# Kernel tuning notes

Hardware: AMD Instinct MI355X
Metric: run time of the kernel (lower is better)

The kernel has to match this reference:

```python
import jax, jax.numpy as jnp
import numpy as np


def _warp(x, flow):
    """Backward bilinear warp (grid_sample equivalent, zeros padding).

    x:    [B, C, H, W] feature frame
    flow: [B, 2, H, W] per-pixel motion vector (x, y) in pixels
    Samples x at (px + flow_x, py + flow_y) with bilinear interpolation;
    out-of-bounds samples contribute zero (padding_mode='zeros').
    """
    B, C, H, W = x.shape
    ys, xs = jnp.meshgrid(jnp.arange(H, dtype=x.dtype), jnp.arange(W, dtype=x.dtype), indexing='ij')
    gx = xs[None] + flow[:, 0]  # [B, H, W] sample x coords
    gy = ys[None] + flow[:, 1]  # [B, H, W] sample y coords
    x0 = jnp.floor(gx)
    y0 = jnp.floor(gy)
    wx = gx - x0
    wy = gy - y0
    flat = x.reshape(B, C, H * W)

    def corner(xi, yi, w):
        valid = (xi >= 0) & (xi <= W - 1) & (yi >= 0) & (yi <= H - 1)
        xc = jnp.clip(xi, 0, W - 1).astype(jnp.int32)
        yc = jnp.clip(yi, 0, H - 1).astype(jnp.int32)
        idx = (yc * W + xc).reshape(B, 1, H * W)
        v = jnp.take_along_axis(flat, idx, axis=2).reshape(B, C, H, W)
        return v * (w * valid.astype(x.dtype))[:, None]

    return (corner(x0, y0, (1.0 - wx) * (1.0 - wy))
            + corner(x0 + 1.0, y0, wx * (1.0 - wy))
            + corner(x0, y0 + 1.0, (1.0 - wx) * wy)
            + corner(x0 + 1.0, y0 + 1.0, wx * wy))


def setup_inputs() -> dict:
    key = jax.random.key(0)
    k1, k2 = jax.random.split(key)
    B, I, C, H, W = 2, 5, 16, 544, 960
    features = jax.random.normal(k1, (B, I, C, H, W), dtype=jnp.float32)
    mv = jax.random.normal(k2, (B, I, 2, H, W), dtype=jnp.float32) * 4.0  # ~4 px motion
    return {"features": features, "mv": mv}


def reference(features, mv):
    """Accumulative backward warp.

    Original torch loop: for i in 1..I-1: for j = i-1 .. 0:
        features[:, i] = warp(features[:, i], mv[:, j])
    i.e. frame i is sequentially warped by mv[i-1], mv[i-2], ..., mv[0].
    Equivalent vectorized form: for j = I-2 .. 0, warp all frames > j by
    mv[:, j] simultaneously (each frame still sees mv indices in descending
    order), removing the per-frame Python loop.
    """
    I = features.shape[1]
    warp_frames = jax.vmap(_warp, in_axes=(1, None), out_axes=1)  # over frame axis
    out = features
    for j in range(I - 2, -1, -1):
        warped = warp_frames(out[:, j + 1:], mv[:, j])  # [B, I-1-j, C, H, W]
        out = out.at[:, j + 1:].set(warped)
    return out
```

## Files before the change

### kernel.cpp

```cpp
#include <hip/hip_runtime.h>
#include <stdint.h>

namespace {
constexpr int Wd = 960, Hd = 544, Cd = 16, Id = 5, Bd = 2;
constexpr int HW = Hd * Wd;
constexpr long CHW = (long)Cd * HW;
constexpr long FRAME_BSTRIDE = (long)Id * CHW;
constexpr long FLOW_BSTRIDE  = (long)Id * 2 * HW;

constexpr int TSX = 64, TSY = 32;
constexpr int HALO = 12;
constexpr int TWX = TSX + 2 * HALO;
constexpr int TWY = TSY + 2 * HALO;
constexpr int NCHUNK = 20;
constexpr int TILE_F = NCHUNK * 256;
constexpr int GX = Wd / TSX;
constexpr int GY = Hd / TSY;
constexpr int NWG = GX * GY * Bd;
}

struct F2 { float x, y; };
struct Job { const float* s; long ss; float* d; long ds; const float* fl; };

__global__ __launch_bounds__(512) void warp_jobs(
    Job j0, Job j1, Job j2, Job j3, Job j4)
{
  __shared__ float tile[2][TILE_F];

  const int jb = blockIdx.y;
  Job J = j0;
  if      (jb == 1) J = j1;
  else if (jb == 2) J = j2;
  else if (jb == 3) J = j3;
  else if (jb == 4) J = j4;

  const int orig = blockIdx.x;
  const int xcd  = orig & 7;
  constexpr int q = NWG / 8, r = NWG % 8;
  const int wgid = (xcd < r ? xcd * (q + 1) : r * (q + 1) + (xcd - r) * q)
                 + (orig >> 3);

  const int b   = wgid / (GX * GY);
  const int rem = wgid - b * (GX * GY);
  const int tyb = rem / GX;
  const int txb = rem - tyb * GX;
  const int X0 = txb * TSX;
  const int Y0 = tyb * TSY;

  const float* sF = J.s + (long)b * J.ss;
  float*       dF = J.d + (long)b * J.ds;

  const int t   = threadIdx.x;
  const int x   = X0 + ((t & 15) << 2);
  const int y   = Y0 + (t >> 4);
  const int pix = y * Wd + x;

  if (J.fl == nullptr) {
#pragma unroll
    for (int c = 0; c < Cd; ++c)
      *reinterpret_cast<float4*>(dF + (long)c * HW + pix)
          = *reinterpret_cast<const float4*>(sF + (long)c * HW + pix);
    return;
  }

  const float* fl = J.fl + (long)b * FLOW_BSTRIDE;
  float4 fxv = *reinterpret_cast<const float4*>(fl + pix);
  float4 fyv = *reinterpret_cast<const float4*>(fl + HW + pix);

  float w00[4], w10[4], w01[4], w11[4];
  int   lA[4];
  int   g00[4], g10[4], g01[4], g11[4];

#pragma unroll
  for (int j = 0; j < 4; ++j) {
    float fx = (j == 0) ? fxv.x : (j == 1) ? fxv.y : (j == 2) ? fxv.z : fxv.w;
    float fy = (j == 0) ? fyv.x : (j == 1) ? fyv.y : (j == 2) ? fyv.z : fyv.w;
    float gx = (float)(x + j) + fx;
    float gy = (float)y + fy;
    float x0f = floorf(gx), y0f = floorf(gy);
    float wx = gx - x0f, wy = gy - y0f;
    bool vx0 = (x0f >= 0.f) && (x0f <= (float)(Wd - 1));
    bool vx1 = (x0f + 1.f >= 0.f) && (x0f + 1.f <= (float)(Wd - 1));
    bool vy0 = (y0f >= 0.f) && (y0f <= (float)(Hd - 1));
    bool vy1 = (y0f + 1.f >= 0.f) && (y0f + 1.f <= (float)(Hd - 1));
    w00[j] = (1.f - wx) * (1.f - wy) * ((vx0 && vy0) ? 1.f : 0.f);
    w10[j] = wx * (1.f - wy)         * ((vx1 && vy0) ? 1.f : 0.f);
    w01[j] = (1.f - wx) * wy         * ((vx0 && vy1) ? 1.f : 0.f);
    w11[j] = wx * wy                 * ((vx1 && vy1) ? 1.f : 0.f);
    int ix0 = (int)x0f;
    int iy0 = (int)y0f;
    int lx = ix0 - (X0 - HALO);
    int ly = iy0 - (Y0 - HALO);
    bool ft = (lx >= 0) & (lx <= TWX - 2) & (ly >= 0) & (ly <= TWY - 2);
    lA[j] = ft ? (ly * TWX + lx) * 4 : -1;
    int xc0 = min(max(ix0, 0), Wd - 1), xc1 = min(max(ix0 + 1, 0), Wd - 1);
    int yc0 = min(max(iy0, 0), Hd - 1), yc1 = min(max(iy0 + 1, 0), Hd - 1);
    g00[j] = yc0 * Wd + xc0;
    g10[j] = yc0 * Wd + xc1;
    g01[j] = yc1 * Wd + xc0;
    g11[j] = yc1 * Wd + xc1;
  }

  const int lane = t & 63;
  const int wv   = t >> 6;
  const int nck  = (wv < 4) ? 3 : 2;
  int goff[3];
#pragma unroll
  for (int k = 0; k < 3; ++k) {
    int ck = wv + 8 * k;
    if (ck < NCHUNK) {
      int foff = ck * 256 + lane * 4;
      int ly = foff / TWX;
      int lx = foff - ly * TWX;
      int gxc = min(max(X0 - HALO + lx, 0), Wd - 4);
      int gyc = min(max(Y0 - HALO + ly, 0), Hd - 1);
      goff[k] = gyc * Wd + gxc;
    }
  }

  auto fill = [&](int nb, const float* sC) {
#pragma unroll
    for (int k = 0; k < 3; ++k) {
      if (k < nck) {
        __builtin_amdgcn_global_load_lds(
            (__attribute__((address_space(1))) void*)(void*)(sC + goff[k]),
            (__attribute__((address_space(3))) void*)&tile[nb][(wv + 8 * k) * 256],
            16, 0, 0);
      }
    }
  };

  fill(0, sF);

#pragma unroll
  for (int c = 0; c < Cd; ++c) {
    __syncthreads();
    if (c + 1 < Cd) fill((c + 1) & 1, sF + (long)(c + 1) * HW);
    const float* sC = sF + (long)c * HW;
    const float* tb = tile[c & 1];
    float ov[4];
#pragma unroll
    for (int j = 0; j < 4; ++j) {
      float v;
      if (lA[j] >= 0) {
        F2 r0 = *(const F2*)((const char*)tb + lA[j]);
        F2 r1 = *(const F2*)((const char*)tb + lA[j] + TWX * 4);
        v = (w00[j] * r0.x + w10[j] * r0.y) + (w01[j] * r1.x + w11[j] * r1.y);
      } else {
        v = w00[j] * sC[g00[j]] + w10[j] * sC[g10[j]]
          + w01[j] * sC[g01[j]] + w11[j] * sC[g11[j]];
      }
      ov[j] = v;
    }
    *reinterpret_cast<float4*>(dF + (long)c * HW + pix)
        = make_float4(ov[0], ov[1], ov[2], ov[3]);
  }
}

extern "C" void kernel_launch(void* const* d_in, const int* in_sizes, int n_in,
                              void* d_out, int out_size, void* d_ws, size_t ws_size,
                              hipStream_t stream) {
  const float* feat = (const float*)d_in[0];
  const float* mv   = (const float*)d_in[1];
  float*       out  = (float*)d_out;
  float*       ws   = (float*)d_ws;

  dim3 block(512, 1, 1);
  const long FB = FRAME_BSTRIDE;
  auto mkjob = [](const float* s, long ss, float* d, long ds, const float* fl) {
    Job j; j.s = s; j.ss = ss; j.d = d; j.ds = ds; j.fl = fl; return j;
  };
  Job Z = mkjob(nullptr, 0, nullptr, 0, nullptr);
  const float* flj[4] = { mv + 0L * 2 * HW, mv + 1L * 2 * HW,
                          mv + 2L * 2 * HW, mv + 3L * 2 * HW };

  auto launch = [&](int nj, Job a, Job b, Job c, Job d, Job e) {
    warp_jobs<<<dim3(NWG, nj, 1), block, 0, stream>>>(a, b, c, d, e);
  };

  const size_t need4 = (size_t)(4 * CHW) * Bd * sizeof(float);
  const size_t need3 = (size_t)(3 * CHW) * Bd * sizeof(float);

  if (ws_size >= need4) {
    const long WB = 4 * CHW;
    float* W0 = ws + 0 * CHW;
    float* W1 = ws + 1 * CHW;
    float* W2 = ws + 2 * CHW;
    float* W3 = ws + 3 * CHW;
    launch(5,
      mkjob(feat + 1 * CHW, FB, out + 1 * CHW, FB, flj[0]),
      mkjob(feat + 2 * CHW, FB, W0, WB, flj[1]),
      mkjob(feat + 3 * CHW, FB, W1, WB, flj[2]),
      mkjob(feat + 4 * CHW, FB, W2, WB, flj[3]),
      mkjob(feat + 0 * CHW, FB, out + 0 * CHW, FB, nullptr));
    launch(3,
      mkjob(W0, WB, out + 2 * CHW, FB, flj[0]),
      mkjob(W1, WB, W3, WB, flj[1]),
      mkjob(W2, WB, out + 4 * CHW, FB, flj[2]), Z, Z);
    launch(2,
      mkjob(W3, WB, out + 3 * CHW, FB, flj[0]),
      mkjob(out + 4 * CHW, FB, W0, WB, flj[1]), Z, Z, Z);
    launch(1, mkjob(W0, WB, out + 4 * CHW, FB, flj[0]), Z, Z, Z, Z);
  } else if (ws_size >= need3) {
    const long WB = 3 * CHW;
    float* W0 = ws + 0 * CHW;
    float* W1 = ws + 1 * CHW;
    float* W2 = ws + 2 * CHW;
    float* S  = out;
    launch(4,
      mkjob(feat + 1 * CHW, FB, out + 1 * CHW, FB, flj[0]),
      mkjob(feat + 2 * CHW, FB, W0, WB, flj[1]),
      mkjob(feat + 3 * CHW, FB, W1, WB, flj[2]),
      mkjob(feat + 4 * CHW, FB, W2, WB, flj[3]), Z);
    launch(3,
      mkjob(W0, WB, out + 2 * CHW, FB, flj[0]),
      mkjob(W1, WB, S, FB, flj[1]),
      mkjob(W2, WB, out + 4 * CHW, FB, flj[2]), Z, Z);
    launch(2,
      mkjob(S, FB, out + 3 * CHW, FB, flj[0]),
      mkjob(out + 4 * CHW, FB, W0, WB, flj[1]), Z, Z, Z);
    launch(1, mkjob(W0, WB, out + 4 * CHW, FB, flj[0]), Z, Z, Z, Z);
    launch(1, mkjob(feat, FB, out, FB, nullptr), Z, Z, Z, Z);
  } else {
    float* S = out;
    auto w1 = [&](const float* s, float* d, int j) {
      launch(1, mkjob(s, FB, d, FB, flj[j]), Z, Z, Z, Z);
    };
    w1(feat + 1 * CHW, out + 1 * CHW, 0);
    w1(feat + 2 * CHW, S, 1);
    w1(S, out + 2 * CHW, 0);
    w1(feat + 3 * CHW, out + 3 * CHW, 2);
    w1(out + 3 * CHW, S, 1);
    w1(S, out + 3 * CHW, 0);
    w1(feat + 4 * CHW, S, 3);
    w1(S, out + 4 * CHW, 2);
    w1(out + 4 * CHW, S, 1);
    w1(S, out + 4 * CHW, 0);
    launch(1, mkjob(feat, FB, out, FB, nullptr), Z, Z, Z, Z);
  }
}
```

Before: 375.0 us.

## Store intermediate warped frames in bf16 workspace to halve traffic

```diff
diff --git a/kernel.cpp b/kernel.cpp
--- a/kernel.cpp
+++ b/kernel.cpp
@@ -20,7 +20,17 @@
 }
 
 struct F2 { float x, y; };
-struct Job { const float* s; long ss; float* d; long ds; const float* fl; };
+struct Job {
+  const void* s; long ss;
+  void*       d; long ds;
+  const float* fl;
+  int sBF, dBF;
+};
+
+__device__ __forceinline__ uint f2bf_bits(float v) {
+  uint x = __float_as_uint(v);
+  return (x + 0x7FFFu + ((x >> 16) & 1u)) >> 16;
+}
 
 __global__ __launch_bounds__(512) void warp_jobs(
     Job j0, Job j1, Job j2, Job j3, Job j4)
@@ -47,19 +57,23 @@
   const int X0 = txb * TSX;
   const int Y0 = tyb * TSY;
 
-  const float* sF = J.s + (long)b * J.ss;
-  float*       dF = J.d + (long)b * J.ds;
-
   const int t   = threadIdx.x;
   const int x   = X0 + ((t & 15) << 2);
   const int y   = Y0 + (t >> 4);
   const int pix = y * Wd + x;
 
+  const float*    sF32 = (const float*)J.s + (long)b * J.ss;
+  float*          dF32 = (float*)J.d + (long)b * J.ds;
+  const uint16_t* sB16 = (const uint16_t*)J.s + (long)b * J.ss;
+  uint16_t*       dB16 = (uint16_t*)J.d + (long)b * J.ds;
+  const bool sBF = J.sBF != 0;
+  const bool dBF = J.dBF != 0;
+
   if (J.fl == nullptr) {
 #pragma unroll
     for (int c = 0; c < Cd; ++c)
-      *reinterpret_cast<float4*>(dF + (long)c * HW + pix)
-          = *reinterpret_cast<const float4*>(sF + (long)c * HW + pix);
+      *reinterpret_cast<float4*>(dF32 + (long)c * HW + pix)
+          = *reinterpret_cast<const float4*>(sF32 + (long)c * HW + pix);
     return;
   }
 
@@ -118,7 +132,8 @@
     }
   }
 
-  auto fill = [&](int nb, const float* sC) {
+  auto fill32 = [&](int nb, int c) {
+    const float* sC = sF32 + (long)c * HW;
 #pragma unroll
     for (int k = 0; k < 3; ++k) {
       if (k < nck) {
@@ -130,13 +145,35 @@
     }
   };
 
-  fill(0, sF);
+  uint2 ld[3];
+  auto loadB = [&](int c) {
+    const uint* gp = (const uint*)(sB16 + (long)c * HW);
+#pragma unroll
+    for (int k = 0; k < 3; ++k)
+      if (k < nck) ld[k] = *(const uint2*)(gp + (goff[k] >> 1));
+  };
+  auto writeB = [&](int nb) {
+#pragma unroll
+    for (int k = 0; k < 3; ++k) {
+      if (k < nck) {
+        float4 f;
+        f.x = __uint_as_float(ld[k].x << 16);
+        f.y = __uint_as_float(ld[k].x & 0xFFFF0000u);
+        f.z = __uint_as_float(ld[k].y << 16);
+        f.w = __uint_as_float(ld[k].y & 0xFFFF0000u);
+        *reinterpret_cast<float4*>(&tile[nb][(wv + 8 * k) * 256 + lane * 4]) = f;
+      }
+    }
+  };
+
+  if (sBF) { loadB(0); writeB(0); } else fill32(0, 0);
 
 #pragma unroll
   for (int c = 0; c < Cd; ++c) {
     __syncthreads();
-    if (c + 1 < Cd) fill((c + 1) & 1, sF + (long)(c + 1) * HW);
-    const float* sC = sF + (long)c * HW;
+    const bool pre = (c + 1 < Cd);
+    if (pre) { if (sBF) loadB(c + 1); else fill32((c + 1) & 1, c + 1); }
+
     const float* tb = tile[c & 1];
     float ov[4];
 #pragma unroll
@@ -146,14 +183,29 @@
         F2 r0 = *(const F2*)((const char*)tb + lA[j]);
         F2 r1 = *(const F2*)((const char*)tb + lA[j] + TWX * 4);
         v = (w00[j] * r0.x + w10[j] * r0.y) + (w01[j] * r1.x + w11[j] * r1.y);
+      } else if (sBF) {
+        const uint16_t* su = sB16 + (long)c * HW;
+        float v00 = __uint_as_float((uint)su[g00[j]] << 16);
+        float v10 = __uint_as_float((uint)su[g10[j]] << 16);
+        float v01 = __uint_as_float((uint)su[g01[j]] << 16);
+        float v11 = __uint_as_float((uint)su[g11[j]] << 16);
+        v = w00[j] * v00 + w10[j] * v10 + w01[j] * v01 + w11[j] * v11;
       } else {
+        const float* sC = sF32 + (long)c * HW;
         v = w00[j] * sC[g00[j]] + w10[j] * sC[g10[j]]
           + w01[j] * sC[g01[j]] + w11[j] * sC[g11[j]];
       }
       ov[j] = v;
     }
-    *reinterpret_cast<float4*>(dF + (long)c * HW + pix)
-        = make_float4(ov[0], ov[1], ov[2], ov[3]);
+    if (dBF) {
+      uint p0 = f2bf_bits(ov[0]) | (f2bf_bits(ov[1]) << 16);
+      uint p1 = f2bf_bits(ov[2]) | (f2bf_bits(ov[3]) << 16);
+      *reinterpret_cast<uint2*>(dB16 + (long)c * HW + pix) = make_uint2(p0, p1);
+    } else {
+      *reinterpret_cast<float4*>(dF32 + (long)c * HW + pix)
+          = make_float4(ov[0], ov[1], ov[2], ov[3]);
+    }
+    if (pre && sBF) writeB((c + 1) & 1);
   }
 }
 
@@ -163,14 +215,15 @@
   const float* feat = (const float*)d_in[0];
   const float* mv   = (const float*)d_in[1];
   float*       out  = (float*)d_out;
-  float*       ws   = (float*)d_ws;
 
   dim3 block(512, 1, 1);
   const long FB = FRAME_BSTRIDE;
-  auto mkjob = [](const float* s, long ss, float* d, long ds, const float* fl) {
-    Job j; j.s = s; j.ss = ss; j.d = d; j.ds = ds; j.fl = fl; return j;
-  };
-  Job Z = mkjob(nullptr, 0, nullptr, 0, nullptr);
+  auto mkjob = [](const void* s, long ss, void* d, long ds, const float* fl,
+                  int sBF, int dBF) {
+    Job j; j.s = s; j.ss = ss; j.d = d; j.ds = ds; j.fl = fl;
+    j.sBF = sBF; j.dBF = dBF; return j;
+  };
+  Job Z = mkjob(nullptr, 0, nullptr, 0, nullptr, 0, 0);
   const float* flj[4] = { mv + 0L * 2 * HW, mv + 1L * 2 * HW,
                           mv + 2L * 2 * HW, mv + 3L * 2 * HW };
 
@@ -178,53 +231,36 @@
     warp_jobs<<<dim3(NWG, nj, 1), block, 0, stream>>>(a, b, c, d, e);
   };
 
-  const size_t need4 = (size_t)(4 * CHW) * Bd * sizeof(float);
-  const size_t need3 = (size_t)(3 * CHW) * Bd * sizeof(float);
-
-  if (ws_size >= need4) {
+  const size_t need = (size_t)(4 * CHW) * Bd * sizeof(uint16_t);
+
+  if (ws_size >= need) {
+    uint16_t* W  = (uint16_t*)d_ws;
     const long WB = 4 * CHW;
-    float* W0 = ws + 0 * CHW;
-    float* W1 = ws + 1 * CHW;
-    float* W2 = ws + 2 * CHW;
-    float* W3 = ws + 3 * CHW;
+    uint16_t* wa = W + 0 * CHW;
+    uint16_t* wb = W + 1 * CHW;
+    uint16_t* wd = W + 2 * CHW;
+    uint16_t* wc = W + 3 * CHW;
+    uint16_t* we = (uint16_t*)(out + 4 * CHW);
+    const long EB = 2 * FB;
+
     launch(5,
-      mkjob(feat + 1 * CHW, FB, out + 1 * CHW, FB, flj[0]),
-      mkjob(feat + 2 * CHW, FB, W0, WB, flj[1]),
-      mkjob(feat + 3 * CHW, FB, W1, WB, flj[2]),
-      mkjob(feat + 4 * CHW, FB, W2, WB, flj[3]),
-      mkjob(feat + 0 * CHW, FB, out + 0 * CHW, FB, nullptr));
+      mkjob(feat + 1 * CHW, FB, out + 1 * CHW, FB, flj[0], 0, 0),
+      mkjob(feat + 2 * CHW, FB, wa, WB, flj[1], 0, 1),
+      mkjob(feat + 3 * CHW, FB, wb, WB, flj[2], 0, 1),
+      mkjob(feat + 4 * CHW, FB, wd, WB, flj[3], 0, 1),
+      mkjob(feat, FB, out, FB, nullptr, 0, 0));
     launch(3,
-      mkjob(W0, WB, out + 2 * CHW, FB, flj[0]),
-      mkjob(W1, WB, W3, WB, flj[1]),
-      mkjob(W2, WB, out + 4 * CHW, FB, flj[2]), Z, Z);
+      mkjob(wa, WB, out + 2 * CHW, FB, flj[0], 1, 0),
+      mkjob(wb, WB, wc, WB, flj[1], 1, 1),
+      mkjob(wd, WB, we, EB, flj[2], 1, 1), Z, Z);
     launch(2,
-      mkjob(W3, WB, out + 3 * CHW, FB, flj[0]),
-      mkjob(out + 4 * CHW, FB, W0, WB, flj[1]), Z, Z, Z);
-    launch(1, mkjob(W0, WB, out + 4 * CHW, FB, flj[0]), Z, Z, Z, Z);
-  } else if (ws_size >= need3) {
-    const long WB = 3 * CHW;
-    float* W0 = ws + 0 * CHW;
-    float* W1 = ws + 1 * CHW;
-    float* W2 = ws + 2 * CHW;
-    float* S  = out;
-    launch(4,
-      mkjob(feat + 1 * CHW, FB, out + 1 * CHW, FB, flj[0]),
-      mkjob(feat + 2 * CHW, FB, W0, WB, flj[1]),
-      mkjob(feat + 3 * CHW, FB, W1, WB, flj[2]),
-      mkjob(feat + 4 * CHW, FB, W2, WB, flj[3]), Z);
-    launch(3,
-      mkjob(W0, WB, out + 2 * CHW, FB, flj[0]),
-      mkjob(W1, WB, S, FB, flj[1]),
-      mkjob(W2, WB, out + 4 * CHW, FB, flj[2]), Z, Z);
-    launch(2,
-      mkjob(S, FB, out + 3 * CHW, FB, flj[0]),
-      mkjob(out + 4 * CHW, FB, W0, WB, flj[1]), Z, Z, Z);
-    launch(1, mkjob(W0, WB, out + 4 * CHW, FB, flj[0]), Z, Z, Z, Z);
-    launch(1, mkjob(feat, FB, out, FB, nullptr), Z, Z, Z, Z);
+      mkjob(wc, WB, out + 3 * CHW, FB, flj[0], 1, 0),
+      mkjob(we, EB, wa, WB, flj[1], 1, 1), Z, Z, Z);
+    launch(1, mkjob(wa, WB, out + 4 * CHW, FB, flj[0], 1, 0), Z, Z, Z, Z);
   } else {
     float* S = out;
     auto w1 = [&](const float* s, float* d, int j) {
-      launch(1, mkjob(s, FB, d, FB, flj[j]), Z, Z, Z, Z);
+      launch(1, mkjob(s, FB, d, FB, flj[j], 0, 0), Z, Z, Z, Z);
     };
     w1(feat + 1 * CHW, out + 1 * CHW, 0);
     w1(feat + 2 * CHW, S, 1);
@@ -236,6 +272,6 @@
     w1(S, out + 4 * CHW, 2);
     w1(out + 4 * CHW, S, 1);
     w1(S, out + 4 * CHW, 0);
-    launch(1, mkjob(feat, FB, out, FB, nullptr), Z, Z, Z, Z);
-  }
-}
+    launch(1, mkjob(feat, FB, out, FB, nullptr, 0, 0), Z, Z, Z, Z);
+  }
+}
```

Result: faster. 339.2 us (-9.5%).
